# Kernel optimization log

Hardware: AMD Instinct MI355X
Metric: run time of the kernel (lower is better)

The kernel has to match this reference:

```python
import jax, jax.numpy as jnp
import numpy as np

SEQ, INPUT_DIM, HIDDEN, CLASSES, BATCH = 2048, 1, 128, 10, 8192


def setup_inputs() -> dict:
    key = jax.random.key(0)
    ks = jax.random.split(key, 6)
    stdv = 1.0 / np.sqrt(HIDDEN).astype(np.float32)
    return {
        "x": jax.random.normal(ks[0], (BATCH, SEQ), dtype=jnp.float32),
        "w_hx": stdv * jax.random.normal(ks[1], (HIDDEN, INPUT_DIM), dtype=jnp.float32),
        "w_hh": stdv * jax.random.normal(ks[2], (HIDDEN, HIDDEN), dtype=jnp.float32),
        "b_h": stdv * jax.random.normal(ks[3], (HIDDEN,), dtype=jnp.float32),
        "w_ph": stdv * jax.random.normal(ks[4], (CLASSES, HIDDEN), dtype=jnp.float32),
        "b_p": stdv * jax.random.normal(ks[5], (CLASSES,), dtype=jnp.float32),
    }


def reference(x, w_hx, w_hh, b_h, w_ph, b_p):
    # x: [B, T] scalar input per timestep (input_dim == 1)
    B = x.shape[0]
    H = w_hh.shape[0]
    xs = x.T  # [T, B], scan over time
    h0 = jnp.zeros((H, B), dtype=x.dtype)

    def step(h, x_t):
        # x_t: [B]; w_hx @ x_t[None, :] -> [H, B]
        h_new = jnp.tanh(w_hx @ x_t[None, :] + w_hh @ h + b_h[:, None])
        return h_new, None

    h_last, _ = jax.lax.scan(step, h0, xs)
    p = w_ph @ h_last + b_p[:, None]  # [C, B]
    return p.T  # [B, C]
```

## Files before the change

kernel.cpp:

```cpp
#include <hip/hip_runtime.h>

typedef int      i32x4 __attribute__((ext_vector_type(4)));
typedef float    f32x4 __attribute__((ext_vector_type(4)));
typedef unsigned u32x2 __attribute__((ext_vector_type(2)));

#define RNN_H 128
#define RNN_T 2048
#define RNN_B 8192
#define RNN_C 10
#define BLK_N 16
#define QSW 32512.0f
#define K2E 2.885390081777927f

#define BAR() asm volatile("s_waitcnt lgkmcnt(0)\n\ts_barrier" ::: "memory")
#define MEMPIN() asm volatile("" ::: "memory")

__device__ __forceinline__ i32x4 mfma_i8(i32x4 a, i32x4 b, i32x4 c) {
  return __builtin_amdgcn_mfma_i32_16x16x64_i8(a, b, c, 0, 0, 0);
}


__global__ __launch_bounds__(256, 2)
void rnn_fused(const float* __restrict__ x, const float* __restrict__ w_hx,
               const float* __restrict__ w_hh, const float* __restrict__ b_h,
               const float* __restrict__ w_ph, const float* __restrict__ b_p,
               float* __restrict__ out)
{
  __shared__ u32x2 hbuf[2][2][2][2][64];
  __shared__ float rs[128];

  const int tid  = threadIdx.x;
  const int lane = tid & 63;
  const int wv   = tid >> 6;
  const int g    = lane >> 4;
  const int l15  = lane & 15;
  const int n0   = blockIdx.x * BLK_N;
  const int sw = wv >> 1, hw = wv & 1, so = sw ^ 1;

  {
    u32x2 z = {0u, 0u};
    u32x2* p = &hbuf[0][0][0][0][0];
    p[tid] = z; p[tid + 256] = z;
  }

  i32x4 WA[2][2], WB[2][2];
  float rm[2];
  #pragma unroll
  for (int mt = 0; mt < 2; ++mt) {
    const float* wrow = w_hh + (size_t)(wv*32 + mt*16 + l15)*RNN_H + 4*g;
    float vals[2][4][4];
    float mx = 0.0f;
    #pragma unroll
    for (int li = 0; li < 2; ++li) {
      const int s = li ? so : sw;
      #pragma unroll
      for (int d = 0; d < 4; ++d) {
        const int jg = li ? d : ((d < 2) ? (2*hw + d) : (2*(hw^1) + (d-2)));
        f32x4 v = *(const f32x4*)(wrow + s*64 + jg*16);
        #pragma unroll
        for (int r = 0; r < 4; ++r) { vals[li][d][r] = v[r]; mx = fmaxf(mx, fabsf(v[r])); }
      }
    }
    mx = fmaxf(mx, __shfl_xor(mx, 16));
    mx = fmaxf(mx, __shfl_xor(mx, 32));
    const float inv = (mx > 0.0f) ? (QSW / mx) : 0.0f;
    rm[mt] = mx * (1.0f / QSW);
    #pragma unroll
    for (int li = 0; li < 2; ++li)
      #pragma unroll
      for (int d = 0; d < 4; ++d) {
        unsigned pa = 0, pb = 0;
        #pragma unroll
        for (int r = 0; r < 4; ++r) {
          const int Wq  = (int)rintf(vals[li][d][r] * inv);
          const int wa  = (Wq + 128) >> 8;
          const int wbv = Wq - (wa << 8);
          pa |= ((unsigned)(wa  & 255)) << (8*r);
          pb |= ((unsigned)(wbv & 255)) << (8*r);
        }
        WA[mt][li][d] = (int)pa;
        WB[mt][li][d] = (int)pb;
      }
  }

  if (g == 0) {
    rs[wv*32 +  0 + l15] = rm[0];
    rs[wv*32 + 16 + l15] = rm[1];
  }
  __syncthreads();

  f32x4 kk2[2], wx2[2], bh2[2];
  #pragma unroll
  for (int mt = 0; mt < 2; ++mt)
    #pragma unroll
    for (int r = 0; r < 4; ++r) {
      const int m = wv*32 + mt*16 + 4*g + r;
      kk2[mt][r] = rs[m] * (K2E / 127.0f);
      wx2[mt][r] = w_hx[m] * K2E;
      bh2[mt][r] = b_h[m] * K2E;
    }

  const float* px = x + (size_t)(n0 + l15) * RNN_T;
  f32x4 xc = *(const f32x4*)px;

  const i32x4 ZI = {0,0,0,0};
  u32x2 ownA = {0u,0u}, ownB = {0u,0u};

  const unsigned c0080 = 0x00800080u;
  const unsigned selA  = 0x07050301u;
  const unsigned selB  = 0x06040200u;
  const float TPP = 32512.0f / 32767.0f;
  const float TPN = -2.0f * TPP;

  __syncthreads();

  for (int t4 = 0; t4 < RNN_T/4; ++t4) {
    f32x4 xn = xc;
    if (t4 + 1 < RNN_T/4) xn = *(const f32x4*)(px + 4*t4 + 4);
    #pragma unroll
    for (int qq = 0; qq < 4; ++qq) {
      const int rb = qq & 1, wb2 = rb ^ 1;
      const float xv = xc[qq];

      const u32x2 poA = hbuf[rb][sw][0][hw^1][lane];
      const u32x2 poB = hbuf[rb][sw][1][hw^1][lane];
      const u32x2 oa0 = hbuf[rb][so][0][0][lane];
      const u32x2 oa1 = hbuf[rb][so][0][1][lane];
      const u32x2 ob0 = hbuf[rb][so][1][0][lane];
      const u32x2 ob1 = hbuf[rb][so][1][1][lane];
      MEMPIN();

      const i32x4 FaOwn = {(int)ownA[0], (int)ownA[1], (int)poA[0], (int)poA[1]};
      const i32x4 FbOwn = {(int)ownB[0], (int)ownB[1], (int)poB[0], (int)poB[1]};
      const i32x4 FaOth = {(int)oa0[0], (int)oa0[1], (int)oa1[0], (int)oa1[1]};
      const i32x4 FbOth = {(int)ob0[0], (int)ob0[1], (int)ob1[0], (int)ob1[1]};

      i32x4 P1[2], P23[2];
      __builtin_amdgcn_s_setprio(1);
      P1[0]  = mfma_i8(WA[0][0], FaOwn, ZI);
      P1[1]  = mfma_i8(WA[1][0], FaOwn, ZI);
      P23[0] = mfma_i8(WB[0][0], FaOwn, ZI);
      P23[1] = mfma_i8(WB[1][0], FaOwn, ZI);
      P23[0] = mfma_i8(WA[0][0], FbOwn, P23[0]);
      P23[1] = mfma_i8(WA[1][0], FbOwn, P23[1]);
      P1[0]  = mfma_i8(WA[0][1], FaOth, P1[0]);
      P1[1]  = mfma_i8(WA[1][1], FaOth, P1[1]);
      P23[0] = mfma_i8(WB[0][1], FaOth, P23[0]);
      P23[1] = mfma_i8(WB[1][1], FaOth, P23[1]);
      P23[0] = mfma_i8(WA[0][1], FbOth, P23[0]);
      P23[1] = mfma_i8(WA[1][1], FbOth, P23[1]);
      __builtin_amdgcn_s_setprio(0);

      unsigned napk[2], nbpk[2];
      #pragma unroll
      for (int mt = 0; mt < 2; ++mt) {
        float tp0, tp1, tp2, tp3;
        {
          const int X0 = (P1[mt][0] << 8) + P23[mt][0];
          const int X1 = (P1[mt][1] << 8) + P23[mt][1];
          const int X2 = (P1[mt][2] << 8) + P23[mt][2];
          const int X3 = (P1[mt][3] << 8) + P23[mt][3];
          const float v0 = __builtin_fmaf(kk2[mt][0], (float)X0,
                             __builtin_fmaf(wx2[mt][0], xv, bh2[mt][0]));
          const float v1 = __builtin_fmaf(kk2[mt][1], (float)X1,
                             __builtin_fmaf(wx2[mt][1], xv, bh2[mt][1]));
          const float v2 = __builtin_fmaf(kk2[mt][2], (float)X2,
                             __builtin_fmaf(wx2[mt][2], xv, bh2[mt][2]));
          const float v3 = __builtin_fmaf(kk2[mt][3], (float)X3,
                             __builtin_fmaf(wx2[mt][3], xv, bh2[mt][3]));
          const float e0 = __builtin_amdgcn_exp2f(v0);
          const float e1 = __builtin_amdgcn_exp2f(v1);
          const float e2 = __builtin_amdgcn_exp2f(v2);
          const float e3 = __builtin_amdgcn_exp2f(v3);
          const float r0 = __builtin_amdgcn_rcpf(e0 + 1.0f);
          const float r1 = __builtin_amdgcn_rcpf(e1 + 1.0f);
          const float r2 = __builtin_amdgcn_rcpf(e2 + 1.0f);
          const float r3 = __builtin_amdgcn_rcpf(e3 + 1.0f);
          tp0 = __builtin_fmaf(r0, TPN, TPP);
          tp1 = __builtin_fmaf(r1, TPN, TPP);
          tp2 = __builtin_fmaf(r2, TPN, TPP);
          tp3 = __builtin_fmaf(r3, TPN, TPP);
        }
        unsigned q01, q23, a01, a23, pa, pb;
        asm("v_cvt_pknorm_i16_f32 %0, %1, %2" : "=v"(q01) : "v"(tp0), "v"(tp1));
        asm("v_cvt_pknorm_i16_f32 %0, %1, %2" : "=v"(q23) : "v"(tp2), "v"(tp3));
        asm("v_pk_add_i16 %0, %1, %2" : "=v"(a01) : "v"(q01), "v"(c0080));
        asm("v_pk_add_i16 %0, %1, %2" : "=v"(a23) : "v"(q23), "v"(c0080));
        asm("v_perm_b32 %0, %1, %2, %3" : "=v"(pa) : "v"(a23), "v"(a01), "v"(selA));
        asm("v_perm_b32 %0, %1, %2, %3" : "=v"(pb) : "v"(q23), "v"(q01), "v"(selB));
        napk[mt] = pa; nbpk[mt] = pb;
      }
      ownA = u32x2{napk[0], napk[1]};
      ownB = u32x2{nbpk[0], nbpk[1]};

      hbuf[wb2][sw][0][hw][lane] = ownA;
      hbuf[wb2][sw][1][hw][lane] = ownB;
      BAR();
    }
    xc = xn;
  }

  __syncthreads();

  {
    const int c = tid >> 4;
    const int n = tid & 15;
    if (c < RNN_C) {
      float sum = b_p[c];
      for (int k = 0; k < RNN_H; ++k) {
        const int s  = k >> 6;
        const int ko = k & 63;
        const int g2 = (ko >> 2) & 3;
        const int j  = (ko & 3) + 4*(ko >> 4);
        const int half = j >> 3, jj = j & 7;
        const signed char* pa = (const signed char*)&hbuf[0][s][0][half][16*g2 + n];
        const signed char* pb = (const signed char*)&hbuf[0][s][1][half][16*g2 + n];
        const int qv = 256*(int)pa[jj] + (int)pb[jj];
        sum = __builtin_fmaf(w_ph[c*RNN_H + k], qv * (1.0f/QSW), sum);
      }
      out[(size_t)(n0 + n)*RNN_C + c] = sum;
    }
  }
}

extern "C" void kernel_launch(void* const* d_in, const int* in_sizes, int n_in,
                              void* d_out, int out_size, void* d_ws, size_t ws_size,
                              hipStream_t stream) {
  (void)in_sizes; (void)n_in; (void)out_size; (void)d_ws; (void)ws_size;
  const float* x    = (const float*)d_in[0];
  const float* w_hx = (const float*)d_in[1];
  const float* w_hh = (const float*)d_in[2];
  const float* b_h  = (const float*)d_in[3];
  const float* w_ph = (const float*)d_in[4];
  const float* b_p  = (const float*)d_in[5];
  float* out = (float*)d_out;
  rnn_fused<<<dim3(RNN_B/BLK_N), dim3(256), 0, stream>>>(x, w_hx, w_hh, b_h, w_ph, b_p, out);
}
```

Measured before the change: 1.005 ms.

## Interleave two batch tiles per block to overlap MFMA with tanh epilogue

```diff
diff --git a/kernel.cpp b/kernel.cpp
--- a/kernel.cpp
+++ b/kernel.cpp
@@ -8,19 +8,19 @@
 #define RNN_T 2048
 #define RNN_B 8192
 #define RNN_C 10
-#define BLK_N 16
+#define BLK_N 32
 #define QSW 32512.0f
 #define K2E 2.885390081777927f
 
 #define BAR() asm volatile("s_waitcnt lgkmcnt(0)\n\ts_barrier" ::: "memory")
-#define MEMPIN() asm volatile("" ::: "memory")
+#define SBAR() __builtin_amdgcn_sched_barrier(0)
 
 __device__ __forceinline__ i32x4 mfma_i8(i32x4 a, i32x4 b, i32x4 c) {
   return __builtin_amdgcn_mfma_i32_16x16x64_i8(a, b, c, 0, 0, 0);
 }
 
 
-__global__ __launch_bounds__(256, 2)
+__global__ __launch_bounds__(256, 1)
 void rnn_fused(const float* __restrict__ x, const float* __restrict__ w_hx,
                const float* __restrict__ w_hh, const float* __restrict__ b_h,
                const float* __restrict__ w_ph, const float* __restrict__ b_p,
@@ -40,7 +40,7 @@
   {
     u32x2 z = {0u, 0u};
     u32x2* p = &hbuf[0][0][0][0][0];
-    p[tid] = z; p[tid + 256] = z;
+    p[tid] = z; p[tid+256] = z; p[tid+512] = z; p[tid+768] = z;
   }
 
   i32x4 WA[2][2], WB[2][2];
@@ -100,11 +100,16 @@
       bh2[mt][r] = b_h[m] * K2E;
     }
 
-  const float* px = x + (size_t)(n0 + l15) * RNN_T;
-  f32x4 xc = *(const f32x4*)px;
+  const float* pxA = x + (size_t)(n0 + l15) * RNN_T;
+  const float* pxB = x + (size_t)(n0 + 16 + l15) * RNN_T;
+  f32x4 xcA = *(const f32x4*)pxA;
+  f32x4 xcB = *(const f32x4*)pxB;
 
   const i32x4 ZI = {0,0,0,0};
-  u32x2 ownA = {0u,0u}, ownB = {0u,0u};
+  u32x2 oAa = {0u,0u}, oAb = {0u,0u}, oBa = {0u,0u}, oBb = {0u,0u};
+  i32x4 pA1[2], pA23[2], pB1[2], pB23[2];
+  #pragma unroll
+  for (int mt = 0; mt < 2; ++mt) { pB1[mt] = ZI; pB23[mt] = ZI; }
 
   const unsigned c0080 = 0x00800080u;
   const unsigned selA  = 0x07050301u;
@@ -114,98 +119,109 @@
 
   __syncthreads();
 
+  auto do_mfma = [&](int TI, const u32x2& ofa, const u32x2& ofb,
+                     i32x4* Pd, i32x4* Pe) {
+    const u32x2 poA = hbuf[TI][sw][0][hw^1][lane];
+    const u32x2 poB = hbuf[TI][sw][1][hw^1][lane];
+    const u32x2 oa0 = hbuf[TI][so][0][0][lane];
+    const u32x2 oa1 = hbuf[TI][so][0][1][lane];
+    const u32x2 ob0 = hbuf[TI][so][1][0][lane];
+    const u32x2 ob1 = hbuf[TI][so][1][1][lane];
+    const i32x4 FaOwn = {(int)ofa[0], (int)ofa[1], (int)poA[0], (int)poA[1]};
+    const i32x4 FbOwn = {(int)ofb[0], (int)ofb[1], (int)poB[0], (int)poB[1]};
+    const i32x4 FaOth = {(int)oa0[0], (int)oa0[1], (int)oa1[0], (int)oa1[1]};
+    const i32x4 FbOth = {(int)ob0[0], (int)ob0[1], (int)ob1[0], (int)ob1[1]};
+    Pd[0] = mfma_i8(WA[0][0], FaOwn, ZI);
+    Pd[1] = mfma_i8(WA[1][0], FaOwn, ZI);
+    Pe[0] = mfma_i8(WB[0][0], FaOwn, ZI);
+    Pe[1] = mfma_i8(WB[1][0], FaOwn, ZI);
+    Pe[0] = mfma_i8(WA[0][0], FbOwn, Pe[0]);
+    Pe[1] = mfma_i8(WA[1][0], FbOwn, Pe[1]);
+    Pd[0] = mfma_i8(WA[0][1], FaOth, Pd[0]);
+    Pd[1] = mfma_i8(WA[1][1], FaOth, Pd[1]);
+    Pe[0] = mfma_i8(WB[0][1], FaOth, Pe[0]);
+    Pe[1] = mfma_i8(WB[1][1], FaOth, Pe[1]);
+    Pe[0] = mfma_i8(WA[0][1], FbOth, Pe[0]);
+    Pe[1] = mfma_i8(WA[1][1], FbOth, Pe[1]);
+  };
+
+  auto do_epi = [&](int TI, const i32x4* Pd, const i32x4* Pe, float xv,
+                    u32x2& ofa, u32x2& ofb) {
+    unsigned napk[2], nbpk[2];
+    #pragma unroll
+    for (int mt = 0; mt < 2; ++mt) {
+      float tp0, tp1, tp2, tp3;
+      {
+        const int X0 = (Pd[mt][0] << 8) + Pe[mt][0];
+        const int X1 = (Pd[mt][1] << 8) + Pe[mt][1];
+        const int X2 = (Pd[mt][2] << 8) + Pe[mt][2];
+        const int X3 = (Pd[mt][3] << 8) + Pe[mt][3];
+        const float v0 = __builtin_fmaf(kk2[mt][0], (float)X0,
+                           __builtin_fmaf(wx2[mt][0], xv, bh2[mt][0]));
+        const float v1 = __builtin_fmaf(kk2[mt][1], (float)X1,
+                           __builtin_fmaf(wx2[mt][1], xv, bh2[mt][1]));
+        const float v2 = __builtin_fmaf(kk2[mt][2], (float)X2,
+                           __builtin_fmaf(wx2[mt][2], xv, bh2[mt][2]));
+        const float v3 = __builtin_fmaf(kk2[mt][3], (float)X3,
+                           __builtin_fmaf(wx2[mt][3], xv, bh2[mt][3]));
+        const float e0 = __builtin_amdgcn_exp2f(v0);
+        const float e1 = __builtin_amdgcn_exp2f(v1);
+        const float e2 = __builtin_amdgcn_exp2f(v2);
+        const float e3 = __builtin_amdgcn_exp2f(v3);
+        const float r0 = __builtin_amdgcn_rcpf(e0 + 1.0f);
+        const float r1 = __builtin_amdgcn_rcpf(e1 + 1.0f);
+        const float r2 = __builtin_amdgcn_rcpf(e2 + 1.0f);
+        const float r3 = __builtin_amdgcn_rcpf(e3 + 1.0f);
+        tp0 = __builtin_fmaf(r0, TPN, TPP);
+        tp1 = __builtin_fmaf(r1, TPN, TPP);
+        tp2 = __builtin_fmaf(r2, TPN, TPP);
+        tp3 = __builtin_fmaf(r3, TPN, TPP);
+      }
+      unsigned q01, q23, a01, a23, pa, pb;
+      asm("v_cvt_pknorm_i16_f32 %0, %1, %2" : "=v"(q01) : "v"(tp0), "v"(tp1));
+      asm("v_cvt_pknorm_i16_f32 %0, %1, %2" : "=v"(q23) : "v"(tp2), "v"(tp3));
+      asm("v_pk_add_i16 %0, %1, %2" : "=v"(a01) : "v"(q01), "v"(c0080));
+      asm("v_pk_add_i16 %0, %1, %2" : "=v"(a23) : "v"(q23), "v"(c0080));
+      asm("v_perm_b32 %0, %1, %2, %3" : "=v"(pa) : "v"(a23), "v"(a01), "v"(selA));
+      asm("v_perm_b32 %0, %1, %2, %3" : "=v"(pb) : "v"(q23), "v"(q01), "v"(selB));
+      napk[mt] = pa; nbpk[mt] = pb;
+    }
+    ofa = u32x2{napk[0], napk[1]};
+    ofb = u32x2{nbpk[0], nbpk[1]};
+    hbuf[TI][sw][0][hw][lane] = ofa;
+    hbuf[TI][sw][1][hw][lane] = ofb;
+  };
+
   for (int t4 = 0; t4 < RNN_T/4; ++t4) {
-    f32x4 xn = xc;
-    if (t4 + 1 < RNN_T/4) xn = *(const f32x4*)(px + 4*t4 + 4);
+    f32x4 xnA = xcA, xnB = xcB;
+    if (t4 + 1 < RNN_T/4) {
+      xnA = *(const f32x4*)(pxA + 4*t4 + 4);
+      xnB = *(const f32x4*)(pxB + 4*t4 + 4);
+    }
     #pragma unroll
     for (int qq = 0; qq < 4; ++qq) {
-      const int rb = qq & 1, wb2 = rb ^ 1;
-      const float xv = xc[qq];
-
-      const u32x2 poA = hbuf[rb][sw][0][hw^1][lane];
-      const u32x2 poB = hbuf[rb][sw][1][hw^1][lane];
-      const u32x2 oa0 = hbuf[rb][so][0][0][lane];
-      const u32x2 oa1 = hbuf[rb][so][0][1][lane];
-      const u32x2 ob0 = hbuf[rb][so][1][0][lane];
-      const u32x2 ob1 = hbuf[rb][so][1][1][lane];
-      MEMPIN();
-
-      const i32x4 FaOwn = {(int)ownA[0], (int)ownA[1], (int)poA[0], (int)poA[1]};
-      const i32x4 FbOwn = {(int)ownB[0], (int)ownB[1], (int)poB[0], (int)poB[1]};
-      const i32x4 FaOth = {(int)oa0[0], (int)oa0[1], (int)oa1[0], (int)oa1[1]};
-      const i32x4 FbOth = {(int)ob0[0], (int)ob0[1], (int)ob1[0], (int)ob1[1]};
-
-      i32x4 P1[2], P23[2];
-      __builtin_amdgcn_s_setprio(1);
-      P1[0]  = mfma_i8(WA[0][0], FaOwn, ZI);
-      P1[1]  = mfma_i8(WA[1][0], FaOwn, ZI);
-      P23[0] = mfma_i8(WB[0][0], FaOwn, ZI);
-      P23[1] = mfma_i8(WB[1][0], FaOwn, ZI);
-      P23[0] = mfma_i8(WA[0][0], FbOwn, P23[0]);
-      P23[1] = mfma_i8(WA[1][0], FbOwn, P23[1]);
-      P1[0]  = mfma_i8(WA[0][1], FaOth, P1[0]);
-      P1[1]  = mfma_i8(WA[1][1], FaOth, P1[1]);
-      P23[0] = mfma_i8(WB[0][1], FaOth, P23[0]);
-      P23[1] = mfma_i8(WB[1][1], FaOth, P23[1]);
-      P23[0] = mfma_i8(WA[0][1], FbOth, P23[0]);
-      P23[1] = mfma_i8(WA[1][1], FbOth, P23[1]);
-      __builtin_amdgcn_s_setprio(0);
-
-      unsigned napk[2], nbpk[2];
-      #pragma unroll
-      for (int mt = 0; mt < 2; ++mt) {
-        float tp0, tp1, tp2, tp3;
-        {
-          const int X0 = (P1[mt][0] << 8) + P23[mt][0];
-          const int X1 = (P1[mt][1] << 8) + P23[mt][1];
-          const int X2 = (P1[mt][2] << 8) + P23[mt][2];
-          const int X3 = (P1[mt][3] << 8) + P23[mt][3];
-          const float v0 = __builtin_fmaf(kk2[mt][0], (float)X0,
-                             __builtin_fmaf(wx2[mt][0], xv, bh2[mt][0]));
-          const float v1 = __builtin_fmaf(kk2[mt][1], (float)X1,
-                             __builtin_fmaf(wx2[mt][1], xv, bh2[mt][1]));
-          const float v2 = __builtin_fmaf(kk2[mt][2], (float)X2,
-                             __builtin_fmaf(wx2[mt][2], xv, bh2[mt][2]));
-          const float v3 = __builtin_fmaf(kk2[mt][3], (float)X3,
-                             __builtin_fmaf(wx2[mt][3], xv, bh2[mt][3]));
-          const float e0 = __builtin_amdgcn_exp2f(v0);
-          const float e1 = __builtin_amdgcn_exp2f(v1);
-          const float e2 = __builtin_amdgcn_exp2f(v2);
-          const float e3 = __builtin_amdgcn_exp2f(v3);
-          const float r0 = __builtin_amdgcn_rcpf(e0 + 1.0f);
-          const float r1 = __builtin_amdgcn_rcpf(e1 + 1.0f);
-          const float r2 = __builtin_amdgcn_rcpf(e2 + 1.0f);
-          const float r3 = __builtin_amdgcn_rcpf(e3 + 1.0f);
-          tp0 = __builtin_fmaf(r0, TPN, TPP);
-          tp1 = __builtin_fmaf(r1, TPN, TPP);
-          tp2 = __builtin_fmaf(r2, TPN, TPP);
-          tp3 = __builtin_fmaf(r3, TPN, TPP);
-        }
-        unsigned q01, q23, a01, a23, pa, pb;
-        asm("v_cvt_pknorm_i16_f32 %0, %1, %2" : "=v"(q01) : "v"(tp0), "v"(tp1));
-        asm("v_cvt_pknorm_i16_f32 %0, %1, %2" : "=v"(q23) : "v"(tp2), "v"(tp3));
-        asm("v_pk_add_i16 %0, %1, %2" : "=v"(a01) : "v"(q01), "v"(c0080));
-        asm("v_pk_add_i16 %0, %1, %2" : "=v"(a23) : "v"(q23), "v"(c0080));
-        asm("v_perm_b32 %0, %1, %2, %3" : "=v"(pa) : "v"(a23), "v"(a01), "v"(selA));
-        asm("v_perm_b32 %0, %1, %2, %3" : "=v"(pb) : "v"(q23), "v"(q01), "v"(selB));
-        napk[mt] = pa; nbpk[mt] = pb;
-      }
-      ownA = u32x2{napk[0], napk[1]};
-      ownB = u32x2{nbpk[0], nbpk[1]};
-
-      hbuf[wb2][sw][0][hw][lane] = ownA;
-      hbuf[wb2][sw][1][hw][lane] = ownB;
+      do_mfma(0, oAa, oAb, pA1, pA23);
+      SBAR();
+      do_epi(1, pB1, pB23, xcB[qq], oBa, oBb);
       BAR();
-    }
-    xc = xn;
+      do_mfma(1, oBa, oBb, pB1, pB23);
+      SBAR();
+      do_epi(0, pA1, pA23, xcA[qq], oAa, oAb);
+      BAR();
+    }
+    xcA = xnA; xcB = xnB;
   }
 
   __syncthreads();
 
-  {
-    const int c = tid >> 4;
-    const int n = tid & 15;
+  #pragma unroll
+  for (int pass = 0; pass < 2; ++pass) {
+    const int idx = tid + pass*256;
+    const int c   = idx >> 5;
+    const int n32 = idx & 31;
     if (c < RNN_C) {
+      const int tile = n32 >> 4;
+      const int n    = n32 & 15;
       float sum = b_p[c];
       for (int k = 0; k < RNN_H; ++k) {
         const int s  = k >> 6;
@@ -213,12 +229,12 @@
         const int g2 = (ko >> 2) & 3;
         const int j  = (ko & 3) + 4*(ko >> 4);
         const int half = j >> 3, jj = j & 7;
-        const signed char* pa = (const signed char*)&hbuf[0][s][0][half][16*g2 + n];
-        const signed char* pb = (const signed char*)&hbuf[0][s][1][half][16*g2 + n];
+        const signed char* pa = (const signed char*)&hbuf[tile][s][0][half][16*g2 + n];
+        const signed char* pb = (const signed char*)&hbuf[tile][s][1][half][16*g2 + n];
         const int qv = 256*(int)pa[jj] + (int)pb[jj];
         sum = __builtin_fmaf(w_ph[c*RNN_H + k], qv * (1.0f/QSW), sum);
       }
-      out[(size_t)(n0 + n)*RNN_C + c] = sum;
+      out[(size_t)(n0 + n32)*RNN_C + c] = sum;
     }
   }
 }
```

Result: slower. 1.739 ms (+73.0%).

## Pack hidden-state A/B planes into 128-bit LDS entries and stagger co-resident blocks

Applied to the files above, without the earlier changes.

```diff
diff --git a/kernel.cpp b/kernel.cpp
--- a/kernel.cpp
+++ b/kernel.cpp
@@ -3,6 +3,7 @@
 typedef int      i32x4 __attribute__((ext_vector_type(4)));
 typedef float    f32x4 __attribute__((ext_vector_type(4)));
 typedef unsigned u32x2 __attribute__((ext_vector_type(2)));
+typedef unsigned u32x4 __attribute__((ext_vector_type(4)));
 
 #define RNN_H 128
 #define RNN_T 2048
@@ -26,7 +27,7 @@
                const float* __restrict__ w_ph, const float* __restrict__ b_p,
                float* __restrict__ out)
 {
-  __shared__ u32x2 hbuf[2][2][2][2][64];
+  __shared__ u32x4 hbuf[2][2][2][64];
   __shared__ float rs[128];
 
   const int tid  = threadIdx.x;
@@ -38,8 +39,8 @@
   const int sw = wv >> 1, hw = wv & 1, so = sw ^ 1;
 
   {
-    u32x2 z = {0u, 0u};
-    u32x2* p = &hbuf[0][0][0][0][0];
+    u32x4 z = {0u, 0u, 0u, 0u};
+    u32x4* p = &hbuf[0][0][0][0];
     p[tid] = z; p[tid + 256] = z;
   }
 
@@ -114,6 +115,13 @@
 
   __syncthreads();
 
+  if (blockIdx.x >= 256) {
+    float acc = (float)lane;
+    #pragma unroll 1
+    for (int i = 0; i < 150; ++i) acc = __builtin_fmaf(acc, 0.9999f, 1.0f);
+    if (acc == 12345.678f) rs[0] = acc;
+  }
+
   for (int t4 = 0; t4 < RNN_T/4; ++t4) {
     f32x4 xn = xc;
     if (t4 + 1 < RNN_T/4) xn = *(const f32x4*)(px + 4*t4 + 4);
@@ -122,18 +130,15 @@
       const int rb = qq & 1, wb2 = rb ^ 1;
       const float xv = xc[qq];
 
-      const u32x2 poA = hbuf[rb][sw][0][hw^1][lane];
-      const u32x2 poB = hbuf[rb][sw][1][hw^1][lane];
-      const u32x2 oa0 = hbuf[rb][so][0][0][lane];
-      const u32x2 oa1 = hbuf[rb][so][0][1][lane];
-      const u32x2 ob0 = hbuf[rb][so][1][0][lane];
-      const u32x2 ob1 = hbuf[rb][so][1][1][lane];
+      const u32x4 RH = hbuf[rb][sw][hw^1][lane];
+      const u32x4 R0 = hbuf[rb][so][0][lane];
+      const u32x4 R1 = hbuf[rb][so][1][lane];
       MEMPIN();
 
-      const i32x4 FaOwn = {(int)ownA[0], (int)ownA[1], (int)poA[0], (int)poA[1]};
-      const i32x4 FbOwn = {(int)ownB[0], (int)ownB[1], (int)poB[0], (int)poB[1]};
-      const i32x4 FaOth = {(int)oa0[0], (int)oa0[1], (int)oa1[0], (int)oa1[1]};
-      const i32x4 FbOth = {(int)ob0[0], (int)ob0[1], (int)ob1[0], (int)ob1[1]};
+      const i32x4 FaOwn = {(int)ownA[0], (int)ownA[1], (int)RH[0], (int)RH[1]};
+      const i32x4 FbOwn = {(int)ownB[0], (int)ownB[1], (int)RH[2], (int)RH[3]};
+      const i32x4 FaOth = {(int)R0[0], (int)R0[1], (int)R1[0], (int)R1[1]};
+      const i32x4 FbOth = {(int)R0[2], (int)R0[3], (int)R1[2], (int)R1[3]};
 
       i32x4 P1[2], P23[2];
       __builtin_amdgcn_s_setprio(1);
@@ -193,8 +198,7 @@
       ownA = u32x2{napk[0], napk[1]};
       ownB = u32x2{nbpk[0], nbpk[1]};
 
-      hbuf[wb2][sw][0][hw][lane] = ownA;
-      hbuf[wb2][sw][1][hw][lane] = ownB;
+      hbuf[wb2][sw][hw][lane] = u32x4{napk[0], napk[1], nbpk[0], nbpk[1]};
       BAR();
     }
     xc = xn;
@@ -213,9 +217,8 @@
         const int g2 = (ko >> 2) & 3;
         const int j  = (ko & 3) + 4*(ko >> 4);
         const int half = j >> 3, jj = j & 7;
-        const signed char* pa = (const signed char*)&hbuf[0][s][0][half][16*g2 + n];
-        const signed char* pb = (const signed char*)&hbuf[0][s][1][half][16*g2 + n];
-        const int qv = 256*(int)pa[jj] + (int)pb[jj];
+        const signed char* base = (const signed char*)&hbuf[0][s][half][16*g2 + n];
+        const int qv = 256*(int)base[jj] + (int)base[8 + jj];
         sum = __builtin_fmaf(w_ph[c*RNN_H + k], qv * (1.0f/QSW), sum);
       }
       out[(size_t)(n0 + n)*RNN_C + c] = sum;
```

Result: slower. 1.056 ms (+5.1%).

## Ping-pong two batch tiles per block to overlap MFMA with epilogue

Applied to the files above, without the earlier changes.

```diff
diff --git a/kernel.cpp b/kernel.cpp
--- a/kernel.cpp
+++ b/kernel.cpp
@@ -8,7 +8,7 @@
 #define RNN_T 2048
 #define RNN_B 8192
 #define RNN_C 10
-#define BLK_N 16
+#define BLK_N 32
 #define QSW 32512.0f
 #define K2E 2.885390081777927f
 
@@ -20,7 +20,7 @@
 }
 
 
-__global__ __launch_bounds__(256, 2)
+__global__ __launch_bounds__(512, 2)
 void rnn_fused(const float* __restrict__ x, const float* __restrict__ w_hx,
                const float* __restrict__ w_hh, const float* __restrict__ b_h,
                const float* __restrict__ w_ph, const float* __restrict__ b_p,
@@ -32,22 +32,24 @@
   const int tid  = threadIdx.x;
   const int lane = tid & 63;
   const int wv   = tid >> 6;
+  const int grp  = wv & 1;
+  const int w4   = wv >> 1;
   const int g    = lane >> 4;
   const int l15  = lane & 15;
   const int n0   = blockIdx.x * BLK_N;
-  const int sw = wv >> 1, hw = wv & 1, so = sw ^ 1;
+  const int sw = w4 >> 1, hw = w4 & 1, so = sw ^ 1;
 
   {
     u32x2 z = {0u, 0u};
     u32x2* p = &hbuf[0][0][0][0][0];
-    p[tid] = z; p[tid + 256] = z;
+    p[tid] = z; p[tid + 512] = z;
   }
 
   i32x4 WA[2][2], WB[2][2];
   float rm[2];
   #pragma unroll
   for (int mt = 0; mt < 2; ++mt) {
-    const float* wrow = w_hh + (size_t)(wv*32 + mt*16 + l15)*RNN_H + 4*g;
+    const float* wrow = w_hh + (size_t)(w4*32 + mt*16 + l15)*RNN_H + 4*g;
     float vals[2][4][4];
     float mx = 0.0f;
     #pragma unroll
@@ -83,9 +85,9 @@
       }
   }
 
-  if (g == 0) {
-    rs[wv*32 +  0 + l15] = rm[0];
-    rs[wv*32 + 16 + l15] = rm[1];
+  if (g == 0 && grp == 0) {
+    rs[w4*32 +  0 + l15] = rm[0];
+    rs[w4*32 + 16 + l15] = rm[1];
   }
   __syncthreads();
 
@@ -94,17 +96,19 @@
   for (int mt = 0; mt < 2; ++mt)
     #pragma unroll
     for (int r = 0; r < 4; ++r) {
-      const int m = wv*32 + mt*16 + 4*g + r;
+      const int m = w4*32 + mt*16 + 4*g + r;
       kk2[mt][r] = rs[m] * (K2E / 127.0f);
       wx2[mt][r] = w_hx[m] * K2E;
       bh2[mt][r] = b_h[m] * K2E;
     }
 
-  const float* px = x + (size_t)(n0 + l15) * RNN_T;
+  const float* px = x + (size_t)(n0 + grp*16 + l15) * RNN_T;
   f32x4 xc = *(const f32x4*)px;
 
   const i32x4 ZI = {0,0,0,0};
   u32x2 ownA = {0u,0u}, ownB = {0u,0u};
+  i32x4 P1[2], P23[2];
+  P1[0] = ZI; P1[1] = ZI; P23[0] = ZI; P23[1] = ZI;
 
   const unsigned c0080 = 0x00800080u;
   const unsigned selA  = 0x07050301u;
@@ -114,88 +118,90 @@
 
   __syncthreads();
 
+  auto do_mfma = [&]() {
+    const u32x2 poA = hbuf[grp][sw][0][hw^1][lane];
+    const u32x2 poB = hbuf[grp][sw][1][hw^1][lane];
+    const u32x2 oa0 = hbuf[grp][so][0][0][lane];
+    const u32x2 oa1 = hbuf[grp][so][0][1][lane];
+    const u32x2 ob0 = hbuf[grp][so][1][0][lane];
+    const u32x2 ob1 = hbuf[grp][so][1][1][lane];
+    MEMPIN();
+    const i32x4 FaOwn = {(int)ownA[0], (int)ownA[1], (int)poA[0], (int)poA[1]};
+    const i32x4 FbOwn = {(int)ownB[0], (int)ownB[1], (int)poB[0], (int)poB[1]};
+    const i32x4 FaOth = {(int)oa0[0], (int)oa0[1], (int)oa1[0], (int)oa1[1]};
+    const i32x4 FbOth = {(int)ob0[0], (int)ob0[1], (int)ob1[0], (int)ob1[1]};
+    __builtin_amdgcn_s_setprio(1);
+    P1[0]  = mfma_i8(WA[0][0], FaOwn, ZI);
+    P1[1]  = mfma_i8(WA[1][0], FaOwn, ZI);
+    P23[0] = mfma_i8(WB[0][0], FaOwn, ZI);
+    P23[1] = mfma_i8(WB[1][0], FaOwn, ZI);
+    P23[0] = mfma_i8(WA[0][0], FbOwn, P23[0]);
+    P23[1] = mfma_i8(WA[1][0], FbOwn, P23[1]);
+    P1[0]  = mfma_i8(WA[0][1], FaOth, P1[0]);
+    P1[1]  = mfma_i8(WA[1][1], FaOth, P1[1]);
+    P23[0] = mfma_i8(WB[0][1], FaOth, P23[0]);
+    P23[1] = mfma_i8(WB[1][1], FaOth, P23[1]);
+    P23[0] = mfma_i8(WA[0][1], FbOth, P23[0]);
+    P23[1] = mfma_i8(WA[1][1], FbOth, P23[1]);
+    __builtin_amdgcn_s_setprio(0);
+  };
+
+  auto do_epi = [&](float xv) {
+    unsigned napk[2], nbpk[2];
+    #pragma unroll
+    for (int mt = 0; mt < 2; ++mt) {
+      float tp0, tp1, tp2, tp3;
+      {
+        const int X0 = (P1[mt][0] << 8) + P23[mt][0];
+        const int X1 = (P1[mt][1] << 8) + P23[mt][1];
+        const int X2 = (P1[mt][2] << 8) + P23[mt][2];
+        const int X3 = (P1[mt][3] << 8) + P23[mt][3];
+        const float v0 = __builtin_fmaf(kk2[mt][0], (float)X0,
+                           __builtin_fmaf(wx2[mt][0], xv, bh2[mt][0]));
+        const float v1 = __builtin_fmaf(kk2[mt][1], (float)X1,
+                           __builtin_fmaf(wx2[mt][1], xv, bh2[mt][1]));
+        const float v2 = __builtin_fmaf(kk2[mt][2], (float)X2,
+                           __builtin_fmaf(wx2[mt][2], xv, bh2[mt][2]));
+        const float v3 = __builtin_fmaf(kk2[mt][3], (float)X3,
+                           __builtin_fmaf(wx2[mt][3], xv, bh2[mt][3]));
+        const float e0 = __builtin_amdgcn_exp2f(v0);
+        const float e1 = __builtin_amdgcn_exp2f(v1);
+        const float e2 = __builtin_amdgcn_exp2f(v2);
+        const float e3 = __builtin_amdgcn_exp2f(v3);
+        const float r0 = __builtin_amdgcn_rcpf(e0 + 1.0f);
+        const float r1 = __builtin_amdgcn_rcpf(e1 + 1.0f);
+        const float r2 = __builtin_amdgcn_rcpf(e2 + 1.0f);
+        const float r3 = __builtin_amdgcn_rcpf(e3 + 1.0f);
+        tp0 = __builtin_fmaf(r0, TPN, TPP);
+        tp1 = __builtin_fmaf(r1, TPN, TPP);
+        tp2 = __builtin_fmaf(r2, TPN, TPP);
+        tp3 = __builtin_fmaf(r3, TPN, TPP);
+      }
+      unsigned q01, q23, a01, a23, pa, pb;
+      asm("v_cvt_pknorm_i16_f32 %0, %1, %2" : "=v"(q01) : "v"(tp0), "v"(tp1));
+      asm("v_cvt_pknorm_i16_f32 %0, %1, %2" : "=v"(q23) : "v"(tp2), "v"(tp3));
+      asm("v_pk_add_i16 %0, %1, %2" : "=v"(a01) : "v"(q01), "v"(c0080));
+      asm("v_pk_add_i16 %0, %1, %2" : "=v"(a23) : "v"(q23), "v"(c0080));
+      asm("v_perm_b32 %0, %1, %2, %3" : "=v"(pa) : "v"(a23), "v"(a01), "v"(selA));
+      asm("v_perm_b32 %0, %1, %2, %3" : "=v"(pb) : "v"(q23), "v"(q01), "v"(selB));
+      napk[mt] = pa; nbpk[mt] = pb;
+    }
+    ownA = u32x2{napk[0], napk[1]};
+    ownB = u32x2{nbpk[0], nbpk[1]};
+    hbuf[grp][sw][0][hw][lane] = ownA;
+    hbuf[grp][sw][1][hw][lane] = ownB;
+  };
+
   for (int t4 = 0; t4 < RNN_T/4; ++t4) {
     f32x4 xn = xc;
     if (t4 + 1 < RNN_T/4) xn = *(const f32x4*)(px + 4*t4 + 4);
     #pragma unroll
     for (int qq = 0; qq < 4; ++qq) {
-      const int rb = qq & 1, wb2 = rb ^ 1;
       const float xv = xc[qq];
-
-      const u32x2 poA = hbuf[rb][sw][0][hw^1][lane];
-      const u32x2 poB = hbuf[rb][sw][1][hw^1][lane];
-      const u32x2 oa0 = hbuf[rb][so][0][0][lane];
-      const u32x2 oa1 = hbuf[rb][so][0][1][lane];
-      const u32x2 ob0 = hbuf[rb][so][1][0][lane];
-      const u32x2 ob1 = hbuf[rb][so][1][1][lane];
-      MEMPIN();
-
-      const i32x4 FaOwn = {(int)ownA[0], (int)ownA[1], (int)poA[0], (int)poA[1]};
-      const i32x4 FbOwn = {(int)ownB[0], (int)ownB[1], (int)poB[0], (int)poB[1]};
-      const i32x4 FaOth = {(int)oa0[0], (int)oa0[1], (int)oa1[0], (int)oa1[1]};
-      const i32x4 FbOth = {(int)ob0[0], (int)ob0[1], (int)ob1[0], (int)ob1[1]};
-
-      i32x4 P1[2], P23[2];
-      __builtin_amdgcn_s_setprio(1);
-      P1[0]  = mfma_i8(WA[0][0], FaOwn, ZI);
-      P1[1]  = mfma_i8(WA[1][0], FaOwn, ZI);
-      P23[0] = mfma_i8(WB[0][0], FaOwn, ZI);
-      P23[1] = mfma_i8(WB[1][0], FaOwn, ZI);
-      P23[0] = mfma_i8(WA[0][0], FbOwn, P23[0]);
-      P23[1] = mfma_i8(WA[1][0], FbOwn, P23[1]);
-      P1[0]  = mfma_i8(WA[0][1], FaOth, P1[0]);
-      P1[1]  = mfma_i8(WA[1][1], FaOth, P1[1]);
-      P23[0] = mfma_i8(WB[0][1], FaOth, P23[0]);
-      P23[1] = mfma_i8(WB[1][1], FaOth, P23[1]);
-      P23[0] = mfma_i8(WA[0][1], FbOth, P23[0]);
-      P23[1] = mfma_i8(WA[1][1], FbOth, P23[1]);
-      __builtin_amdgcn_s_setprio(0);
-
-      unsigned napk[2], nbpk[2];
-      #pragma unroll
-      for (int mt = 0; mt < 2; ++mt) {
-        float tp0, tp1, tp2, tp3;
-        {
-          const int X0 = (P1[mt][0] << 8) + P23[mt][0];
-          const int X1 = (P1[mt][1] << 8) + P23[mt][1];
-          const int X2 = (P1[mt][2] << 8) + P23[mt][2];
-          const int X3 = (P1[mt][3] << 8) + P23[mt][3];
-          const float v0 = __builtin_fmaf(kk2[mt][0], (float)X0,
-                             __builtin_fmaf(wx2[mt][0], xv, bh2[mt][0]));
-          const float v1 = __builtin_fmaf(kk2[mt][1], (float)X1,
-                             __builtin_fmaf(wx2[mt][1], xv, bh2[mt][1]));
-          const float v2 = __builtin_fmaf(kk2[mt][2], (float)X2,
-                             __builtin_fmaf(wx2[mt][2], xv, bh2[mt][2]));
-          const float v3 = __builtin_fmaf(kk2[mt][3], (float)X3,
-                             __builtin_fmaf(wx2[mt][3], xv, bh2[mt][3]));
-          const float e0 = __builtin_amdgcn_exp2f(v0);
-          const float e1 = __builtin_amdgcn_exp2f(v1);
-          const float e2 = __builtin_amdgcn_exp2f(v2);
-          const float e3 = __builtin_amdgcn_exp2f(v3);
-          const float r0 = __builtin_amdgcn_rcpf(e0 + 1.0f);
-          const float r1 = __builtin_amdgcn_rcpf(e1 + 1.0f);
-          const float r2 = __builtin_amdgcn_rcpf(e2 + 1.0f);
-          const float r3 = __builtin_amdgcn_rcpf(e3 + 1.0f);
-          tp0 = __builtin_fmaf(r0, TPN, TPP);
-          tp1 = __builtin_fmaf(r1, TPN, TPP);
-          tp2 = __builtin_fmaf(r2, TPN, TPP);
-          tp3 = __builtin_fmaf(r3, TPN, TPP);
-        }
-        unsigned q01, q23, a01, a23, pa, pb;
-        asm("v_cvt_pknorm_i16_f32 %0, %1, %2" : "=v"(q01) : "v"(tp0), "v"(tp1));
-        asm("v_cvt_pknorm_i16_f32 %0, %1, %2" : "=v"(q23) : "v"(tp2), "v"(tp3));
-        asm("v_pk_add_i16 %0, %1, %2" : "=v"(a01) : "v"(q01), "v"(c0080));
-        asm("v_pk_add_i16 %0, %1, %2" : "=v"(a23) : "v"(q23), "v"(c0080));
-        asm("v_perm_b32 %0, %1, %2, %3" : "=v"(pa) : "v"(a23), "v"(a01), "v"(selA));
-        asm("v_perm_b32 %0, %1, %2, %3" : "=v"(pb) : "v"(q23), "v"(q01), "v"(selB));
-        napk[mt] = pa; nbpk[mt] = pb;
-      }
-      ownA = u32x2{napk[0], napk[1]};
-      ownB = u32x2{nbpk[0], nbpk[1]};
-
-      hbuf[wb2][sw][0][hw][lane] = ownA;
-      hbuf[wb2][sw][1][hw][lane] = ownB;
+      if (grp == 0) do_mfma(); else do_epi(xv);
       BAR();
+      if (grp == 0) do_epi(xv); else do_mfma();
+      BAR();
     }
     xc = xn;
   }
@@ -203,9 +209,11 @@
   __syncthreads();
 
   {
-    const int c = tid >> 4;
-    const int n = tid & 15;
+    const int c   = tid >> 5;
+    const int n32 = tid & 31;
     if (c < RNN_C) {
+      const int tile = n32 >> 4;
+      const int n    = n32 & 15;
       float sum = b_p[c];
       for (int k = 0; k < RNN_H; ++k) {
         const int s  = k >> 6;
@@ -213,12 +221,12 @@
         const int g2 = (ko >> 2) & 3;
         const int j  = (ko & 3) + 4*(ko >> 4);
         const int half = j >> 3, jj = j & 7;
-        const signed char* pa = (const signed char*)&hbuf[0][s][0][half][16*g2 + n];
-        const signed char* pb = (const signed char*)&hbuf[0][s][1][half][16*g2 + n];
+        const signed char* pa = (const signed char*)&hbuf[tile][s][0][half][16*g2 + n];
+        const signed char* pb = (const signed char*)&hbuf[tile][s][1][half][16*g2 + n];
         const int qv = 256*(int)pa[jj] + (int)pb[jj];
         sum = __builtin_fmaf(w_ph[c*RNN_H + k], qv * (1.0f/QSW), sum);
       }
-      out[(size_t)(n0 + n)*RNN_C + c] = sum;
+      out[(size_t)(n0 + n32)*RNN_C + c] = sum;
     }
   }
 }
@@ -234,5 +242,5 @@
   const float* w_ph = (const float*)d_in[4];
   const float* b_p  = (const float*)d_in[5];
   float* out = (float*)d_out;
-  rnn_fused<<<dim3(RNN_B/BLK_N), dim3(256), 0, stream>>>(x, w_hx, w_hh, b_h, w_ph, b_p, out);
+  rnn_fused<<<dim3(RNN_B/BLK_N), dim3(512), 0, stream>>>(x, w_hx, w_hh, b_h, w_ph, b_p, out);
 }
```

Result: slower. 1.540 ms (+53.3%).
